# Performance work log

Hardware: AMD Instinct MI355X
Metric: run time of the kernel (lower is better)

The kernel has to match this reference:

```python
import jax, jax.numpy as jnp
import numpy as np

EPS = 1e-6      # VN division epsilon
BN_EPS = 1e-5   # torch BatchNorm default eps
K = 20          # knn neighbors (vn_get_graph_feature default)


def vn_linear(W, x):
    # W: [out,in]; x: [B,in,3,...] -> [B,out,3,...]
    return jnp.einsum('oc,bc...->bo...', W, x)


def vn_batchnorm(x, gamma, beta):
    # x: [B,C,3,...]; batch-normalize the vector norms (training-mode batch stats)
    norm = jnp.sqrt(jnp.sum(x * x, axis=2)) + EPS          # [B,C,...]
    axes = (0,) + tuple(range(2, norm.ndim))
    mean = jnp.mean(norm, axis=axes, keepdims=True)
    var = jnp.mean((norm - mean) ** 2, axis=axes, keepdims=True)
    shp = (1, -1) + (1,) * (norm.ndim - 2)
    norm_bn = gamma.reshape(shp) * (norm - mean) / jnp.sqrt(var + BN_EPS) + beta.reshape(shp)
    return x * jnp.expand_dims(norm_bn / norm, 2)


def vn_leaky(p, d):
    # VN LeakyReLU with negative_slope = 0.0
    dot = jnp.sum(p * d, axis=2, keepdims=True)
    dsq = jnp.sum(d * d, axis=2, keepdims=True)
    return jnp.where(dot >= 0, p, p - (dot / (dsq + EPS)) * d)


def vn_block(x, W, D, gamma, beta):
    # VNLinearBNLeakyReLU: feat-linear -> VN batchnorm -> VN leaky-relu w/ dir-linear
    p = vn_batchnorm(vn_linear(W, x), gamma, beta)
    return vn_leaky(p, vn_linear(D, x))


def graph_feature(x):
    # x: [B,N,3] points -> VN edge features [B, 3ch, 3vec, N, K]
    sq = jnp.sum(x * x, axis=-1)                            # [B,N]
    inner = jnp.einsum('bnc,bmc->bnm', x, x)                # [B,N,N]
    neg_dist = 2.0 * inner - sq[:, :, None] - sq[:, None, :]  # -||xi-xj||^2
    idx = jax.lax.top_k(neg_dist, K)[1]                     # [B,N,K]
    nbr = jnp.take_along_axis(x[:, None, :, :], idx[..., None], axis=2)  # [B,N,K,3]
    ctr = jnp.broadcast_to(x[:, :, None, :], nbr.shape)     # [B,N,K,3]
    cross = jnp.cross(nbr, ctr)                             # torch.cross(feature, x)
    feat = jnp.stack([nbr - ctr, ctr, cross], axis=3)       # [B,N,K,3ch,3vec]
    return jnp.transpose(feat, (0, 3, 4, 1, 2))


def setup_inputs():
    key = jax.random.key(0)
    ks = jax.random.split(key, 24)
    def lin(k, o, i):
        return jax.random.normal(k, (o, i), jnp.float32) / np.float32(np.sqrt(i))
    def gam(k, c):
        return 1.0 + 0.1 * jax.random.normal(k, (c,), jnp.float32)
    def bet(k, c):
        return 0.1 * jax.random.normal(k, (c,), jnp.float32)
    B, N, feat_dim = 4, 4096, 1024
    inp = {'x': jax.random.normal(ks[0], (B, N, 3), jnp.float32)}
    inp.update(W1=lin(ks[1], 64, 3), D1=lin(ks[2], 64, 3), g1=gam(ks[3], 64), b1=bet(ks[4], 64))
    inp.update(W2=lin(ks[5], 64, 64), D2=lin(ks[6], 64, 64), g2=gam(ks[7], 64), b2=bet(ks[8], 64))
    inp.update(W3=lin(ks[9], 64, 64), D3=lin(ks[10], 64, 64), g3=gam(ks[11], 64), b3=bet(ks[12], 64))
    inp.update(W4=lin(ks[13], 128, 64), D4=lin(ks[14], 128, 64), g4=gam(ks[15], 128), b4=bet(ks[16], 128))
    inp.update(W5=lin(ks[17], feat_dim, 128), g5=gam(ks[18], feat_dim), b5=bet(ks[19], feat_dim))
    return inp


def reference(x, W1, D1, g1, b1, W2, D2, g2, b2, W3, D3, g3, b3, W4, D4, g4, b4, W5, g5, b5):
    f = graph_feature(x)                          # [B,3,3,N,K]
    h = vn_block(f, W1, D1, g1, b1)               # [B,64,3,N,K]
    h = jnp.mean(h, axis=-1)                      # pool1: mean over K -> [B,64,3,N]
    h = vn_block(h, W2, D2, g2, b2)
    h = vn_block(h, W3, D3, g3, b3)
    h = vn_block(h, W4, D4, g4, b4)               # [B,128,3,N]
    h = vn_batchnorm(vn_linear(W5, h), g5, b5)    # conv5 + bn5 -> [B,feat_dim,3,N]
    return jnp.mean(h, axis=-1)                   # pool2 (global_feat): [B,feat_dim,3]
```

## Files before the change

kernel.cpp:

```cpp
#include <hip/hip_runtime.h>
#include <math.h>

#define NB 4
#define NP 4096
#define KNB 20
#define VEPS 1e-6f
#define BNEPS 1e-5f

__global__ void zero_kernel(float* a, int na, float* b, int nb) {
  int i = blockIdx.x * 256 + threadIdx.x;
  if (i < na) a[i] = 0.f;
  if (i < nb) b[i] = 0.f;
}

__global__ __launch_bounds__(256) void knn_kernel(const float* __restrict__ x,
                                                  int* __restrict__ idxout) {
  __shared__ float sx[NP], sy[NP], sz[NP];
  const int b = blockIdx.x >> 7;
  const int blk = blockIdx.x & 127;
  const float* xb = x + b * NP * 3;
  for (int e = threadIdx.x; e < NP * 3; e += 256) {
    float v = xb[e];
    int p = e / 3;
    int c = e - p * 3;
    if (c == 0) sx[p] = v; else if (c == 1) sy[p] = v; else sz[p] = v;
  }
  __syncthreads();
  const int wave = threadIdx.x >> 6, lane = threadIdx.x & 63;
#pragma unroll 1
  for (int q = 0; q < 8; ++q) {
    const int n = blk * 32 + wave * 8 + q;
    const float qx = sx[n], qy = sy[n], qz = sz[n];
    const float sqq = qx * qx + qy * qy + qz * qz;
    unsigned ku[64];
#pragma unroll
    for (int t = 0; t < 64; ++t) {
      int j = t * 64 + lane;
      float px = sx[j], py = sy[j], pz = sz[j];
      float inner = qx * px + qy * py + qz * pz;
      float sqj = px * px + py * py + pz * pz;
      float d = 2.0f * inner - sqq - sqj;
      unsigned u = __float_as_uint(d);
      ku[t] = (u & 0x80000000u) ? ~u : (u | 0x80000000u);
    }
    unsigned p = 0u;
#pragma unroll 1
    for (int bit = 31; bit >= 0; --bit) {
      const unsigned cand = p | (1u << bit);
      int c = 0;
#pragma unroll
      for (int t = 0; t < 64; ++t) c += (ku[t] >= cand) ? 1 : 0;
#pragma unroll
      for (int s = 32; s; s >>= 1) c += __shfl_xor(c, s, 64);
      if (c >= KNB) p = cand;
    }
    const unsigned V = p;
    int cgt = 0;
#pragma unroll
    for (int t = 0; t < 64; ++t) cgt += (ku[t] > V) ? 1 : 0;
    int incl = cgt;
#pragma unroll
    for (int s = 1; s < 64; s <<= 1) {
      int o = __shfl_up(incl, s, 64);
      if (lane >= s) incl += o;
    }
    const int n_gt = __shfl(incl, 63, 64);
    int w = incl - cgt;
    int* outp = idxout + (b * NP + n) * KNB;
#pragma unroll
    for (int t = 0; t < 64; ++t) {
      if (ku[t] > V) { outp[w] = t * 64 + lane; ++w; }
    }
    int lastj = -1;
#pragma unroll 1
    for (int r = n_gt; r < KNB; ++r) {
      int mn = 0x7FFFFFFF;
#pragma unroll
      for (int t = 0; t < 64; ++t) {
        int jt = t * 64 + lane;
        bool el = (ku[t] == V) && (jt > lastj);
        mn = el ? min(mn, jt) : mn;
      }
#pragma unroll
      for (int s = 32; s; s >>= 1) mn = min(mn, __shfl_xor(mn, s, 64));
      if (lane == 0) outp[r] = mn;
      lastj = mn;
    }
  }
}

__global__ __launch_bounds__(256) void bn1_stats_kernel(const float* __restrict__ x,
                                                        const int* __restrict__ idx,
                                                        const float* __restrict__ W1,
                                                        float* __restrict__ stats) {
  const int lane = threadIdx.x & 63, wave = threadIdx.x >> 6;
  const int gw = blockIdx.x * 4 + wave;
  const float w0 = W1[lane * 3 + 0], w1 = W1[lane * 3 + 1], w2 = W1[lane * 3 + 2];
  float s = 0.f, ss = 0.f;
  const int NI = NB * NP * KNB;
  for (int item = gw; item < NI; item += 1024) {
    int b = item / (NP * KNB);
    int r = item - b * (NP * KNB);
    int n = r / KNB;
    int j = idx[item];
    const float* cp = x + (b * NP + n) * 3;
    const float* pp = x + (b * NP + j) * 3;
    float cx = cp[0], cy = cp[1], cz = cp[2];
    float nx = pp[0], ny = pp[1], nz = pp[2];
    float ux = nx - cx, uy = ny - cy, uz = nz - cz;
    float wx = ny * cz - nz * cy, wy = nz * cx - nx * cz, wz = nx * cy - ny * cx;
    float px = w0 * ux + w1 * cx + w2 * wx;
    float py = w0 * uy + w1 * cy + w2 * wy;
    float pz = w0 * uz + w1 * cz + w2 * wz;
    float nm = sqrtf(px * px + py * py + pz * pz) + VEPS;
    s += nm; ss += nm * nm;
  }
  __shared__ float red[2][4][64];
  red[0][wave][lane] = s; red[1][wave][lane] = ss;
  __syncthreads();
  if (wave == 0) {
    float a = red[0][0][lane] + red[0][1][lane] + red[0][2][lane] + red[0][3][lane];
    float c = red[1][0][lane] + red[1][1][lane] + red[1][2][lane] + red[1][3][lane];
    atomicAdd(&stats[lane], a);
    atomicAdd(&stats[64 + lane], c);
  }
}

__global__ void bn_finalize_kernel(float* stage, const float* __restrict__ gamma,
                                   int C, float invcnt) {
  int c = blockIdx.x * 256 + threadIdx.x;
  if (c >= C) return;
  float mean = stage[c] * invcnt;
  float var = stage[C + c] * invcnt - mean * mean;
  var = fmaxf(var, 0.f);
  stage[2 * C + c] = gamma[c] / sqrtf(var + BNEPS);
  stage[3 * C + c] = mean;
}

__global__ __launch_bounds__(256) void block1_apply_kernel(
    const float* __restrict__ x, const int* __restrict__ idx,
    const float* __restrict__ W1, const float* __restrict__ D1,
    const float* __restrict__ stats, const float* __restrict__ beta,
    float* __restrict__ hout) {
  const int lane = threadIdx.x & 63, wave = threadIdx.x >> 6;
  const int b = blockIdx.x >> 8;
  const int nbase = (blockIdx.x & 255) * 16;
  const float w0 = W1[lane * 3], w1 = W1[lane * 3 + 1], w2 = W1[lane * 3 + 2];
  const float e0 = D1[lane * 3], e1 = D1[lane * 3 + 1], e2 = D1[lane * 3 + 2];
  const float sc = stats[128 + lane], mn = stats[192 + lane], be = beta[lane];
  __shared__ float lds[64 * 3 * 17];
#pragma unroll 1
  for (int q = 0; q < 4; ++q) {
    int nl = wave * 4 + q;
    int n = nbase + nl;
    const float* cp = x + (b * NP + n) * 3;
    float cx = cp[0], cy = cp[1], cz = cp[2];
    const int* ip = idx + (b * NP + n) * KNB;
    float ax = 0.f, ay = 0.f, az = 0.f;
    for (int k = 0; k < KNB; ++k) {
      int j = ip[k];
      const float* pp = x + (b * NP + j) * 3;
      float nx = pp[0], ny = pp[1], nz = pp[2];
      float ux = nx - cx, uy = ny - cy, uz = nz - cz;
      float wx = ny * cz - nz * cy, wy = nz * cx - nx * cz, wz = nx * cy - ny * cx;
      float px = w0 * ux + w1 * cx + w2 * wx;
      float py = w0 * uy + w1 * cy + w2 * wy;
      float pz = w0 * uz + w1 * cz + w2 * wz;
      float dx = e0 * ux + e1 * cx + e2 * wx;
      float dy = e0 * uy + e1 * cy + e2 * wy;
      float dz = e0 * uz + e1 * cz + e2 * wz;
      float nm = sqrtf(px * px + py * py + pz * pz) + VEPS;
      float fac = (sc * (nm - mn) + be) / nm;
      px *= fac; py *= fac; pz *= fac;
      float dot = px * dx + py * dy + pz * dz;
      if (dot < 0.f) {
        float tt = dot / (dx * dx + dy * dy + dz * dz + VEPS);
        px -= tt * dx; py -= tt * dy; pz -= tt * dz;
      }
      ax += px; ay += py; az += pz;
    }
    const float k1 = 1.f / (float)KNB;
    lds[(lane * 3 + 0) * 17 + nl] = ax * k1;
    lds[(lane * 3 + 1) * 17 + nl] = ay * k1;
    lds[(lane * 3 + 2) * 17 + nl] = az * k1;
  }
  __syncthreads();
  float* ob = hout + (size_t)(b * 64 * 3) * NP + nbase;
  for (int i = 0; i < 12; ++i) {
    int flat = i * 256 + threadIdx.x;
    int ni = flat & 15, cv = flat >> 4;
    ob[(size_t)cv * NP + ni] = lds[cv * 17 + ni];
  }
}

__device__ __forceinline__ void fma_step(const float* __restrict__ wls,
                                         const float* __restrict__ hs,
                                         int k, int co0, int nl0,
                                         float (&acc)[4][3][4]) {
  float4 wa = *(const float4*)&wls[k * 64 + (co0 ^ ((k & 15) << 2))];
  float4 h0 = *(const float4*)&hs[(k * 3 + 0) * 64 + nl0];
  float4 h1 = *(const float4*)&hs[(k * 3 + 1) * 64 + nl0];
  float4 h2 = *(const float4*)&hs[(k * 3 + 2) * 64 + nl0];
  const float* wv = (const float*)&wa;
  const float* a0 = (const float*)&h0;
  const float* a1 = (const float*)&h1;
  const float* a2 = (const float*)&h2;
#pragma unroll
  for (int ci = 0; ci < 4; ++ci) {
#pragma unroll
    for (int nj = 0; nj < 4; ++nj) {
      acc[ci][0][nj] = fmaf(wv[ci], a0[nj], acc[ci][0][nj]);
      acc[ci][1][nj] = fmaf(wv[ci], a1[nj], acc[ci][1][nj]);
      acc[ci][2][nj] = fmaf(wv[ci], a2[nj], acc[ci][2][nj]);
    }
  }
}

template <int CIN, int COUT, int PHASE>
__global__ __launch_bounds__(256) void vn_gemm_kernel(
    const float* __restrict__ h, const float* __restrict__ Wp,
    const float* __restrict__ Wd, float* __restrict__ stage,
    const float* __restrict__ beta, float* __restrict__ out) {
  __shared__ float hs[64 * 3 * 64];
  __shared__ float wls[64 * 64];
  const int t = threadIdx.x;
  const int b = blockIdx.z;
  const int n0 = blockIdx.x * 64;
  const int cobase = blockIdx.y * 64;
  const int ng = t & 15;
  const int co0 = (t >> 4) * 4;
  const int nl0 = ng * 4;

  float accp[4][3][4] = {};
  float accd[4][3][4] = {};

  for (int chunk = 0; chunk < CIN / 64; ++chunk) {
    const int kb = chunk * 64;
    const float* hbase = h + ((size_t)(b * CIN + kb) * 3) * NP + n0;
    __syncthreads();
#pragma unroll
    for (int i = 0; i < 12; ++i) {
      int flat = i * 256 + t;
      int row = flat >> 4;
      int c4 = (flat & 15) * 4;
      *(float4*)&hs[row * 64 + c4] = *(const float4*)&hbase[(size_t)row * NP + c4];
    }
    {
      const float* Ws = (PHASE == 1) ? Wd : Wp;
#pragma unroll
      for (int i = 0; i < 16; ++i) {
        int flat = i * 256 + t;
        int co = flat >> 6, k = flat & 63;
        wls[k * 64 + (co ^ ((k & 15) << 2))] = Ws[(cobase + co) * CIN + kb + k];
      }
    }
    __syncthreads();
    if (PHASE == 1) {
#pragma unroll 2
      for (int k = 0; k < 64; ++k) fma_step(wls, hs, k, co0, nl0, accd);
      __syncthreads();
#pragma unroll
      for (int i = 0; i < 16; ++i) {
        int flat = i * 256 + t;
        int co = flat >> 6, k = flat & 63;
        wls[k * 64 + (co ^ ((k & 15) << 2))] = Wp[(cobase + co) * CIN + kb + k];
      }
      __syncthreads();
    }
#pragma unroll 2
    for (int k = 0; k < 64; ++k) fma_step(wls, hs, k, co0, nl0, accp);
  }

  if (PHASE == 0) {
#pragma unroll
    for (int ci = 0; ci < 4; ++ci) {
      float s = 0.f, ss = 0.f;
#pragma unroll
      for (int nj = 0; nj < 4; ++nj) {
        float nsq = accp[ci][0][nj] * accp[ci][0][nj] +
                    accp[ci][1][nj] * accp[ci][1][nj] +
                    accp[ci][2][nj] * accp[ci][2][nj];
        float nm = sqrtf(nsq) + VEPS;
        s += nm; ss += nm * nm;
      }
#pragma unroll
      for (int m = 1; m < 16; m <<= 1) {
        s += __shfl_xor(s, m, 64);
        ss += __shfl_xor(ss, m, 64);
      }
      if (ng == 0) {
        atomicAdd(&stage[cobase + co0 + ci], s);
        atomicAdd(&stage[COUT + cobase + co0 + ci], ss);
      }
    }
  } else if (PHASE == 1) {
#pragma unroll
    for (int ci = 0; ci < 4; ++ci) {
      const int ch = cobase + co0 + ci;
      const float sc = stage[2 * COUT + ch], mn = stage[3 * COUT + ch], be = beta[ch];
#pragma unroll
      for (int nj = 0; nj < 4; ++nj) {
        float px = accp[ci][0][nj], py = accp[ci][1][nj], pz = accp[ci][2][nj];
        float nm = sqrtf(px * px + py * py + pz * pz) + VEPS;
        float fac = (sc * (nm - mn) + be) / nm;
        px *= fac; py *= fac; pz *= fac;
        float dx = accd[ci][0][nj], dy = accd[ci][1][nj], dz = accd[ci][2][nj];
        float dot = px * dx + py * dy + pz * dz;
        if (dot < 0.f) {
          float tt = dot / (dx * dx + dy * dy + dz * dz + VEPS);
          px -= tt * dx; py -= tt * dy; pz -= tt * dz;
        }
        accp[ci][0][nj] = px; accp[ci][1][nj] = py; accp[ci][2][nj] = pz;
      }
#pragma unroll
      for (int v = 0; v < 3; ++v) {
        float4 o;
        o.x = accp[ci][v][0]; o.y = accp[ci][v][1];
        o.z = accp[ci][v][2]; o.w = accp[ci][v][3];
        *(float4*)&out[((size_t)(b * COUT + ch) * 3 + v) * NP + n0 + nl0] = o;
      }
    }
  } else {
    const float invN = 1.f / (float)NP;
#pragma unroll
    for (int ci = 0; ci < 4; ++ci) {
      const int ch = cobase + co0 + ci;
      const float sc = stage[2 * COUT + ch], mn = stage[3 * COUT + ch], be = beta[ch];
      float p0 = 0.f, p1 = 0.f, p2 = 0.f;
#pragma unroll
      for (int nj = 0; nj < 4; ++nj) {
        float px = accp[ci][0][nj], py = accp[ci][1][nj], pz = accp[ci][2][nj];
        float nm = sqrtf(px * px + py * py + pz * pz) + VEPS;
        float fac = (sc * (nm - mn) + be) / nm;
        p0 += px * fac; p1 += py * fac; p2 += pz * fac;
      }
#pragma unroll
      for (int m = 1; m < 16; m <<= 1) {
        p0 += __shfl_xor(p0, m, 64);
        p1 += __shfl_xor(p1, m, 64);
        p2 += __shfl_xor(p2, m, 64);
      }
      if (ng == 0) {
        atomicAdd(&out[(size_t)(b * COUT + ch) * 3 + 0], p0 * invN);
        atomicAdd(&out[(size_t)(b * COUT + ch) * 3 + 1], p1 * invN);
        atomicAdd(&out[(size_t)(b * COUT + ch) * 3 + 2], p2 * invN);
      }
    }
  }
}

extern "C" void kernel_launch(void* const* d_in, const int* in_sizes, int n_in,
                              void* d_out, int out_size, void* d_ws, size_t ws_size,
                              hipStream_t stream) {
  const float* x  = (const float*)d_in[0];
  const float* W1 = (const float*)d_in[1];
  const float* D1 = (const float*)d_in[2];
  const float* g1 = (const float*)d_in[3];
  const float* b1 = (const float*)d_in[4];
  const float* W2 = (const float*)d_in[5];
  const float* D2 = (const float*)d_in[6];
  const float* g2 = (const float*)d_in[7];
  const float* b2 = (const float*)d_in[8];
  const float* W3 = (const float*)d_in[9];
  const float* D3 = (const float*)d_in[10];
  const float* g3 = (const float*)d_in[11];
  const float* b3 = (const float*)d_in[12];
  const float* W4 = (const float*)d_in[13];
  const float* D4 = (const float*)d_in[14];
  const float* g4 = (const float*)d_in[15];
  const float* b4 = (const float*)d_in[16];
  const float* W5 = (const float*)d_in[17];
  const float* g5 = (const float*)d_in[18];
  const float* b5 = (const float*)d_in[19];
  float* outp = (float*)d_out;

  char* ws = (char*)d_ws;
  size_t off = 0;
  int* idxw = (int*)(ws + off); off += 4ull * NB * NP * KNB;
  off = (off + 255) & ~255ull;
  float* stats = (float*)(ws + off); off += 4ull * 20480;
  off = (off + 255) & ~255ull;
  float* hA = (float*)(ws + off); off += 4ull * NB * 64 * 3 * NP;
  off = (off + 255) & ~255ull;
  float* hB = (float*)(ws + off); off += 4ull * NB * 128 * 3 * NP;

  float* st1 = stats;
  float* st2 = stats + 4096;
  float* st3 = stats + 8192;
  float* st4 = stats + 12288;
  float* st5 = stats + 16384;

  zero_kernel<<<80, 256, 0, stream>>>(outp, out_size, stats, 20480);
  knn_kernel<<<NB * 128, 256, 0, stream>>>(x, idxw);

  bn1_stats_kernel<<<256, 256, 0, stream>>>(x, idxw, W1, st1);
  bn_finalize_kernel<<<1, 64, 0, stream>>>(st1, g1, 64, 1.f / (float)(NB * NP * KNB));
  block1_apply_kernel<<<NB * 256, 256, 0, stream>>>(x, idxw, W1, D1, st1, b1, hA);

  vn_gemm_kernel<64, 64, 0><<<dim3(64, 1, NB), 256, 0, stream>>>(hA, W2, nullptr, st2, nullptr, nullptr);
  bn_finalize_kernel<<<1, 64, 0, stream>>>(st2, g2, 64, 1.f / (float)(NB * NP));
  vn_gemm_kernel<64, 64, 1><<<dim3(64, 1, NB), 256, 0, stream>>>(hA, W2, D2, st2, b2, hB);

  vn_gemm_kernel<64, 64, 0><<<dim3(64, 1, NB), 256, 0, stream>>>(hB, W3, nullptr, st3, nullptr, nullptr);
  bn_finalize_kernel<<<1, 64, 0, stream>>>(st3, g3, 64, 1.f / (float)(NB * NP));
  vn_gemm_kernel<64, 64, 1><<<dim3(64, 1, NB), 256, 0, stream>>>(hB, W3, D3, st3, b3, hA);

  vn_gemm_kernel<64, 128, 0><<<dim3(64, 2, NB), 256, 0, stream>>>(hA, W4, nullptr, st4, nullptr, nullptr);
  bn_finalize_kernel<<<1, 128, 0, stream>>>(st4, g4, 128, 1.f / (float)(NB * NP));
  vn_gemm_kernel<64, 128, 1><<<dim3(64, 2, NB), 256, 0, stream>>>(hA, W4, D4, st4, b4, hB);

  vn_gemm_kernel<128, 1024, 0><<<dim3(64, 16, NB), 256, 0, stream>>>(hB, W5, nullptr, st5, nullptr, nullptr);
  bn_finalize_kernel<<<4, 256, 0, stream>>>(st5, g5, 1024, 1.f / (float)(NB * NP));
  vn_gemm_kernel<128, 1024, 2><<<dim3(64, 16, NB), 256, 0, stream>>>(hB, W5, nullptr, st5, b5, outp);
}
```

Before: 1.305 ms.

## Speed up kNN radix select by compacting candidates after top byte

The 32-bit radix select for the k-th largest distance key now runs only its first 8 bits over all 64 keys per lane. It then compacts each lane's few keys that fall in the selected top-byte bin into six registers and finishes the remaining 24 bits on those alone, with the count above the bin folded in. If any lane has more than six such keys, it falls back to the full scan. The counting loops are split into eight independent accumulators to shorten dependency chains, and the launch bounds request two blocks per CU, which may pressure the 64-key register array.

```diff
diff --git a/kernel.cpp b/kernel.cpp
--- a/kernel.cpp
+++ b/kernel.cpp
@@ -13,8 +13,42 @@
   if (i < nb) b[i] = 0.f;
 }
 
-__global__ __launch_bounds__(256) void knn_kernel(const float* __restrict__ x,
-                                                  int* __restrict__ idxout) {
+__device__ __forceinline__ void emit_topk(const unsigned (&ku)[64], unsigned V,
+                                          int lane, int* __restrict__ outp) {
+  int cgt = 0;
+#pragma unroll
+  for (int t = 0; t < 64; ++t) cgt += (ku[t] > V) ? 1 : 0;
+  int incl = cgt;
+#pragma unroll
+  for (int s = 1; s < 64; s <<= 1) {
+    int o = __shfl_up(incl, s, 64);
+    if (lane >= s) incl += o;
+  }
+  const int n_gt = __shfl(incl, 63, 64);
+  int w = incl - cgt;
+#pragma unroll
+  for (int t = 0; t < 64; ++t) {
+    if (ku[t] > V) { outp[w] = t * 64 + lane; ++w; }
+  }
+  int lastj = -1;
+#pragma unroll 1
+  for (int r = n_gt; r < KNB; ++r) {
+    int mn = 0x7FFFFFFF;
+#pragma unroll
+    for (int t = 0; t < 64; ++t) {
+      int jt = t * 64 + lane;
+      bool el = (ku[t] == V) && (jt > lastj);
+      mn = el ? min(mn, jt) : mn;
+    }
+#pragma unroll
+    for (int s = 32; s; s >>= 1) mn = min(mn, __shfl_xor(mn, s, 64));
+    if (lane == 0) outp[r] = mn;
+    lastj = mn;
+  }
+}
+
+__global__ __launch_bounds__(256, 2) void knn_kernel(const float* __restrict__ x,
+                                                     int* __restrict__ idxout) {
   __shared__ float sx[NP], sy[NP], sz[NP];
   const int b = blockIdx.x >> 7;
   const int blk = blockIdx.x & 127;
@@ -45,47 +79,89 @@
     }
     unsigned p = 0u;
 #pragma unroll 1
-    for (int bit = 31; bit >= 0; --bit) {
+    for (int bit = 31; bit >= 24; --bit) {
       const unsigned cand = p | (1u << bit);
-      int c = 0;
-#pragma unroll
-      for (int t = 0; t < 64; ++t) c += (ku[t] >= cand) ? 1 : 0;
+      int a0 = 0, a1 = 0, a2 = 0, a3 = 0, a4 = 0, a5 = 0, a6 = 0, a7 = 0;
+#pragma unroll
+      for (int k = 0; k < 8; ++k) {
+        a0 += (ku[0 * 8 + k] >= cand) ? 1 : 0;
+        a1 += (ku[1 * 8 + k] >= cand) ? 1 : 0;
+        a2 += (ku[2 * 8 + k] >= cand) ? 1 : 0;
+        a3 += (ku[3 * 8 + k] >= cand) ? 1 : 0;
+        a4 += (ku[4 * 8 + k] >= cand) ? 1 : 0;
+        a5 += (ku[5 * 8 + k] >= cand) ? 1 : 0;
+        a6 += (ku[6 * 8 + k] >= cand) ? 1 : 0;
+        a7 += (ku[7 * 8 + k] >= cand) ? 1 : 0;
+      }
+      int c = ((a0 + a1) + (a2 + a3)) + ((a4 + a5) + (a6 + a7));
 #pragma unroll
       for (int s = 32; s; s >>= 1) c += __shfl_xor(c, s, 64);
       if (c >= KNB) p = cand;
     }
-    const unsigned V = p;
-    int cgt = 0;
-#pragma unroll
-    for (int t = 0; t < 64; ++t) cgt += (ku[t] > V) ? 1 : 0;
-    int incl = cgt;
-#pragma unroll
-    for (int s = 1; s < 64; s <<= 1) {
-      int o = __shfl_up(incl, s, 64);
-      if (lane >= s) incl += o;
-    }
-    const int n_gt = __shfl(incl, 63, 64);
-    int w = incl - cgt;
-    int* outp = idxout + (b * NP + n) * KNB;
+    const unsigned binTop = p | 0x00FFFFFFu;
+    int h0 = 0, h1 = 0, h2 = 0, h3 = 0, h4 = 0, h5 = 0, h6 = 0, h7 = 0;
+#pragma unroll
+    for (int k = 0; k < 8; ++k) {
+      h0 += (ku[0 * 8 + k] > binTop) ? 1 : 0;
+      h1 += (ku[1 * 8 + k] > binTop) ? 1 : 0;
+      h2 += (ku[2 * 8 + k] > binTop) ? 1 : 0;
+      h3 += (ku[3 * 8 + k] > binTop) ? 1 : 0;
+      h4 += (ku[4 * 8 + k] > binTop) ? 1 : 0;
+      h5 += (ku[5 * 8 + k] > binTop) ? 1 : 0;
+      h6 += (ku[6 * 8 + k] > binTop) ? 1 : 0;
+      h7 += (ku[7 * 8 + k] > binTop) ? 1 : 0;
+    }
+    int cntAbove = ((h0 + h1) + (h2 + h3)) + ((h4 + h5) + (h6 + h7));
+#pragma unroll
+    for (int s = 32; s; s >>= 1) cntAbove += __shfl_xor(cntAbove, s, 64);
+    unsigned s0 = 0u, s1 = 0u, s2 = 0u, s3 = 0u, s4 = 0u, s5 = 0u;
+    int ns = 0;
 #pragma unroll
     for (int t = 0; t < 64; ++t) {
-      if (ku[t] > V) { outp[w] = t * 64 + lane; ++w; }
-    }
-    int lastj = -1;
-#pragma unroll 1
-    for (int r = n_gt; r < KNB; ++r) {
-      int mn = 0x7FFFFFFF;
-#pragma unroll
-      for (int t = 0; t < 64; ++t) {
-        int jt = t * 64 + lane;
-        bool el = (ku[t] == V) && (jt > lastj);
-        mn = el ? min(mn, jt) : mn;
-      }
-#pragma unroll
-      for (int s = 32; s; s >>= 1) mn = min(mn, __shfl_xor(mn, s, 64));
-      if (lane == 0) outp[r] = mn;
-      lastj = mn;
-    }
+      const unsigned v = ku[t];
+      const bool el = (v >= p) && (v <= binTop);
+      s0 = (el && ns == 0) ? v : s0;
+      s1 = (el && ns == 1) ? v : s1;
+      s2 = (el && ns == 2) ? v : s2;
+      s3 = (el && ns == 3) ? v : s3;
+      s4 = (el && ns == 4) ? v : s4;
+      s5 = (el && ns == 5) ? v : s5;
+      ns += el ? 1 : 0;
+    }
+    if (__all(ns <= 6)) {
+#pragma unroll 1
+      for (int bit = 23; bit >= 0; --bit) {
+        const unsigned cand = p | (1u << bit);
+        int c = ((s0 >= cand) ? 1 : 0) + ((s1 >= cand) ? 1 : 0) +
+                ((s2 >= cand) ? 1 : 0) + ((s3 >= cand) ? 1 : 0) +
+                ((s4 >= cand) ? 1 : 0) + ((s5 >= cand) ? 1 : 0);
+#pragma unroll
+        for (int s = 32; s; s >>= 1) c += __shfl_xor(c, s, 64);
+        if (c + cntAbove >= KNB) p = cand;
+      }
+    } else {
+#pragma unroll 1
+      for (int bit = 23; bit >= 0; --bit) {
+        const unsigned cand = p | (1u << bit);
+        int a0 = 0, a1 = 0, a2 = 0, a3 = 0, a4 = 0, a5 = 0, a6 = 0, a7 = 0;
+#pragma unroll
+        for (int k = 0; k < 8; ++k) {
+          a0 += (ku[0 * 8 + k] >= cand) ? 1 : 0;
+          a1 += (ku[1 * 8 + k] >= cand) ? 1 : 0;
+          a2 += (ku[2 * 8 + k] >= cand) ? 1 : 0;
+          a3 += (ku[3 * 8 + k] >= cand) ? 1 : 0;
+          a4 += (ku[4 * 8 + k] >= cand) ? 1 : 0;
+          a5 += (ku[5 * 8 + k] >= cand) ? 1 : 0;
+          a6 += (ku[6 * 8 + k] >= cand) ? 1 : 0;
+          a7 += (ku[7 * 8 + k] >= cand) ? 1 : 0;
+        }
+        int c = ((a0 + a1) + (a2 + a3)) + ((a4 + a5) + (a6 + a7));
+#pragma unroll
+        for (int s = 32; s; s >>= 1) c += __shfl_xor(c, s, 64);
+        if (c >= KNB) p = cand;
+      }
+    }
+    emit_topk(ku, p, lane, idxout + (b * NP + n) * KNB);
   }
 }
 
```

New measurement: 1.365 ms. +4.5%, slower.
